# Performance work log

Measured on AMD Instinct MI355X. Metric: run time of the kernel, lower is better.

## Reference

```python
import jax, jax.numpy as jnp
import numpy as np

H = 64
VOCAB = 64
SLOTS = 8
EPS = 1e-5


def _layernorm(x, gamma, beta):
    mu = jnp.mean(x, axis=-1, keepdims=True)
    var = jnp.mean(jnp.square(x - mu), axis=-1, keepdims=True)
    return (x - mu) * jax.lax.rsqrt(var + EPS) * gamma + beta


def setup_inputs() -> dict:
    key = jax.random.key(0)
    ks = jax.random.split(key, 20)
    B, L = 1024, 2048
    s = 0.05
    inp = {
        "seq": jax.random.randint(ks[0], (B, L), 0, VOCAB, dtype=jnp.int64),
        "embed": jax.random.normal(ks[1], (VOCAB, H), jnp.float32) * s,
        "w1": jax.random.normal(ks[2], (2 * H, H), jnp.float32) * s,
        "b1": jnp.zeros((2 * H,), jnp.float32),
        "w2": jax.random.normal(ks[3], (H, 2 * H), jnp.float32) * s,
        "b2": jnp.zeros((H,), jnp.float32),
        "gamma": jnp.ones((H,), jnp.float32),
        "beta": jnp.zeros((H,), jnp.float32),
        "gate_w": jax.random.normal(ks[4], (1, H), jnp.float32) * s,
        "gate_b": jnp.zeros((1,), jnp.float32),
        "qi_w": jax.random.normal(ks[5], (H, H), jnp.float32) * s,
        "qi_b": jnp.zeros((H,), jnp.float32),
        "sk_w": jax.random.normal(ks[6], (H, H), jnp.float32) * s,
        "sk_b": jnp.zeros((H,), jnp.float32),
        "qr_w": jax.random.normal(ks[7], (H, H), jnp.float32) * s,
        "qr_b": jnp.zeros((H,), jnp.float32),
        "out_w": jax.random.normal(ks[8], (VOCAB, H), jnp.float32) * s,
        "out_b": jnp.zeros((VOCAB,), jnp.float32),
    }
    return inp


def reference(seq, embed, w1, b1, w2, b2, gamma, beta, gate_w, gate_b,
              qi_w, qi_b, sk_w, sk_b, qr_w, qr_b, out_w, out_b):
    # Encoder: embed -> FF residual -> LayerNorm
    h0 = embed[seq]                                  # [B, L, H]
    ff = jax.nn.relu(h0 @ w1.T + b1) @ w2.T + b2     # [B, L, H]
    h = _layernorm(h0 + ff, gamma, beta)             # [B, L, H]

    # Top-k gate over sequence -> gather memory slots
    scores = jnp.squeeze(h @ gate_w.T, -1) + gate_b[0]   # [B, L]
    _, idx = jax.lax.top_k(scores, SLOTS)                # [B, S]
    memory = jnp.take_along_axis(h, idx[:, :, None], axis=1)  # [B, S, H]

    scale = 1.0 / jnp.sqrt(jnp.float32(H))

    # Stage 1: initial read attention over slot keys
    q_init = h[:, -1, :] @ qi_w.T + qi_b                 # [B, H]
    slot_keys = memory @ sk_w.T + sk_b                   # [B, S, H]
    r_attn = jax.nn.softmax(jnp.einsum('bsh,bh->bs', slot_keys, q_init) * scale, axis=-1)
    read = jnp.einsum('bs,bsh->bh', r_attn, memory)
    q_refined = q_init + (read @ qr_w.T + qr_b)          # [B, H]

    # Stage 2: refined attention directly over memory
    attn = jax.nn.softmax(jnp.einsum('bsh,bh->bs', memory, q_refined) * scale, axis=-1)
    pooled = jnp.einsum('bs,bsh->bh', attn, memory)      # [B, H]
    return pooled @ out_w.T + out_b                      # [B, VOCAB]
```

## Files before the change

kernel.cpp:

```cpp
#include <hip/hip_runtime.h>
#include <hip/hip_bf16.h>

#define HD 64
#define LSEQ 2048
#define NBATCH 1024
#define NSLOTS 8

__global__ __launch_bounds__(128) void build_tables_kernel(
    const float* __restrict__ embed, const float* __restrict__ w1, const float* __restrict__ b1,
    const float* __restrict__ w2, const float* __restrict__ b2,
    const float* __restrict__ gamma, const float* __restrict__ beta,
    const float* __restrict__ gate_w, const float* __restrict__ gate_b,
    const float* __restrict__ qi_w, const float* __restrict__ qi_b,
    const float* __restrict__ sk_w, const float* __restrict__ sk_b,
    const float* __restrict__ qr_w, const float* __restrict__ out_w,
    float* __restrict__ h_table, float* __restrict__ qi_table, float* __restrict__ sk_table,
    float* __restrict__ qr_wT, float* __restrict__ out_wT, float* __restrict__ score)
{
    const int blk = blockIdx.x;
    const int tid = threadIdx.x;

    if (blk >= 64) {
        const float* src = (blk == 64) ? qr_w : out_w;
        float*       dst = (blk == 64) ? qr_wT : out_wT;
        for (int i = tid; i < HD * HD; i += 128) {
            int r = i >> 6, c = i & 63;
            dst[c * HD + r] = src[i];
        }
        return;
    }

    const int v = blk;
    __shared__ float E[HD];
    __shared__ float T1[2 * HD];
    __shared__ float Hrow[HD];

    if (tid < HD) E[tid] = embed[v * HD + tid];
    __syncthreads();

    {
        float t1 = b1[tid];
        const float* w1r = w1 + tid * HD;
        #pragma unroll 8
        for (int k = 0; k < HD; ++k) t1 = fmaf(E[k], w1r[k], t1);
        T1[tid] = fmaxf(t1, 0.0f);
    }
    __syncthreads();

    if (tid < HD) {
        float x = E[tid] + b2[tid];
        const float* w2r = w2 + tid * 2 * HD;
        #pragma unroll 8
        for (int j = 0; j < 2 * HD; ++j) x = fmaf(T1[j], w2r[j], x);

        float mu = x;
        #pragma unroll
        for (int off = 1; off < 64; off <<= 1) mu += __shfl_xor(mu, off);
        mu *= (1.0f / 64.0f);
        float d = x - mu;
        float var = d * d;
        #pragma unroll
        for (int off = 1; off < 64; off <<= 1) var += __shfl_xor(var, off);
        var *= (1.0f / 64.0f);
        float h = d * rsqrtf(var + 1e-5f) * gamma[tid] + beta[tid];
        Hrow[tid] = h;
        h_table[v * HD + tid] = h;

        float sc = h * gate_w[tid];
        #pragma unroll
        for (int off = 1; off < 64; off <<= 1) sc += __shfl_xor(sc, off);
        if (tid == 0) score[v] = sc + gate_b[0];
    }
    __syncthreads();

    {
        const int i = tid & 63;
        const float* W  = (tid < HD) ? qi_w : sk_w;
        const float* Bv = (tid < HD) ? qi_b : sk_b;
        float acc = Bv[i];
        const float* Wr = W + i * HD;
        #pragma unroll 8
        for (int k = 0; k < HD; ++k) acc = fmaf(Hrow[k], Wr[k], acc);
        float* dst = (tid < HD) ? qi_table : sk_table;
        dst[v * HD + i] = acc;
    }
}

__global__ __launch_bounds__(64) void sort_tokens_kernel(const float* __restrict__ score,
                                                         int* __restrict__ order)
{
    const int t = threadIdx.x;
    const float st = score[t];
    int rank = 0;
    for (int u = 0; u < 64; ++u) {
        float su = score[u];
        if (su > st || (su == st && u < t)) rank++;
    }
    order[rank] = t;
}

__global__ __launch_bounds__(64) void main_kernel(
    const int* __restrict__ seq,
    const float* __restrict__ h_table, const float* __restrict__ qi_table,
    const float* __restrict__ sk_table, const float* __restrict__ qr_wT,
    const float* __restrict__ qr_b, const float* __restrict__ out_wT,
    const float* __restrict__ out_b, const int* __restrict__ order,
    float* __restrict__ out)
{
    const int b    = blockIdx.x;
    const int lane = threadIdx.x;

    __shared__ int   hist[64];
    __shared__ int   slot_tok[NSLOTS];
    __shared__ float rbuf[64];

    hist[lane] = 0;
    __syncthreads();

    const int*  srow  = seq + (size_t)b * LSEQ;
    const int4* srow4 = (const int4*)srow;
    #pragma unroll
    for (int it = 0; it < LSEQ / 64 / 4; ++it) {
        int4 t4 = srow4[lane + it * 64];
        atomicAdd(&hist[t4.x], 1);
        atomicAdd(&hist[t4.y], 1);
        atomicAdd(&hist[t4.z], 1);
        atomicAdd(&hist[t4.w], 1);
    }
    __syncthreads();

    if (lane == 0) {
        int rem = NSLOTS, pos = 0;
        for (int t = 0; t < 64 && rem > 0; ++t) {
            int tok = order[t];
            int m = hist[tok];
            if (m > rem) m = rem;
            for (int i = 0; i < m; ++i) slot_tok[pos++] = tok;
            rem -= m;
        }
    }
    __syncthreads();

    int st[NSLOTS];
    #pragma unroll
    for (int s = 0; s < NSLOTS; ++s) st[s] = slot_tok[s];

    const int last = srow[LSEQ - 1];
    const float qk = qi_table[last * HD + lane];

    float mrow[NSLOTS], skrow[NSLOTS];
    #pragma unroll
    for (int s = 0; s < NSLOTS; ++s) {
        mrow[s]  = h_table[st[s] * HD + lane];
        skrow[s] = sk_table[st[s] * HD + lane];
    }

    const float scale = 0.125f;

    float p[NSLOTS];
    #pragma unroll
    for (int s = 0; s < NSLOTS; ++s) p[s] = skrow[s] * qk;
    #pragma unroll
    for (int off = 1; off < 64; off <<= 1) {
        #pragma unroll
        for (int s = 0; s < NSLOTS; ++s) p[s] += __shfl_xor(p[s], off);
    }
    {
        float mx = p[0];
        #pragma unroll
        for (int s = 1; s < NSLOTS; ++s) mx = fmaxf(mx, p[s]);
        float sum = 0.0f;
        #pragma unroll
        for (int s = 0; s < NSLOTS; ++s) { p[s] = __expf((p[s] - mx) * scale * 1.0f); }
        (void)sum;
    }
    #pragma unroll
    for (int s = 0; s < NSLOTS; ++s) p[s] = skrow[s] * qk;
    #pragma unroll
    for (int off = 1; off < 64; off <<= 1) {
        #pragma unroll
        for (int s = 0; s < NSLOTS; ++s) p[s] += __shfl_xor(p[s], off);
    }
    #pragma unroll
    for (int s = 0; s < NSLOTS; ++s) p[s] *= scale;
    float r[NSLOTS];
    {
        float mx = p[0];
        #pragma unroll
        for (int s = 1; s < NSLOTS; ++s) mx = fmaxf(mx, p[s]);
        float sum = 0.0f;
        #pragma unroll
        for (int s = 0; s < NSLOTS; ++s) { r[s] = expf(p[s] - mx); sum += r[s]; }
        float inv = 1.0f / sum;
        #pragma unroll
        for (int s = 0; s < NSLOTS; ++s) r[s] *= inv;
    }

    float readk = 0.0f;
    #pragma unroll
    for (int s = 0; s < NSLOTS; ++s) readk = fmaf(r[s], mrow[s], readk);

    rbuf[lane] = readk;
    __syncthreads();

    float qref = qk + qr_b[lane];
    #pragma unroll 4
    for (int j = 0; j < HD; ++j) qref = fmaf(rbuf[j], qr_wT[j * HD + lane], qref);

    float p2[NSLOTS];
    #pragma unroll
    for (int s = 0; s < NSLOTS; ++s) p2[s] = mrow[s] * qref;
    #pragma unroll
    for (int off = 1; off < 64; off <<= 1) {
        #pragma unroll
        for (int s = 0; s < NSLOTS; ++s) p2[s] += __shfl_xor(p2[s], off);
    }
    #pragma unroll
    for (int s = 0; s < NSLOTS; ++s) p2[s] *= scale;
    float a[NSLOTS];
    {
        float mx = p2[0];
        #pragma unroll
        for (int s = 1; s < NSLOTS; ++s) mx = fmaxf(mx, p2[s]);
        float sum = 0.0f;
        #pragma unroll
        for (int s = 0; s < NSLOTS; ++s) { a[s] = expf(p2[s] - mx); sum += a[s]; }
        float inv = 1.0f / sum;
        #pragma unroll
        for (int s = 0; s < NSLOTS; ++s) a[s] *= inv;
    }

    float pooledk = 0.0f;
    #pragma unroll
    for (int s = 0; s < NSLOTS; ++s) pooledk = fmaf(a[s], mrow[s], pooledk);

    __syncthreads();
    rbuf[lane] = pooledk;
    __syncthreads();

    float acc = out_b[lane];
    #pragma unroll 4
    for (int k = 0; k < HD; ++k) acc = fmaf(rbuf[k], out_wT[k * HD + lane], acc);

    out[(size_t)b * HD + lane] = acc;
}

extern "C" void kernel_launch(void* const* d_in, const int* in_sizes, int n_in,
                              void* d_out, int out_size, void* d_ws, size_t ws_size,
                              hipStream_t stream) {
    const int*   seq    = (const int*)  d_in[0];
    const float* embed  = (const float*)d_in[1];
    const float* w1     = (const float*)d_in[2];
    const float* b1     = (const float*)d_in[3];
    const float* w2     = (const float*)d_in[4];
    const float* b2     = (const float*)d_in[5];
    const float* gamma  = (const float*)d_in[6];
    const float* beta   = (const float*)d_in[7];
    const float* gate_w = (const float*)d_in[8];
    const float* gate_b = (const float*)d_in[9];
    const float* qi_w   = (const float*)d_in[10];
    const float* qi_b   = (const float*)d_in[11];
    const float* sk_w   = (const float*)d_in[12];
    const float* sk_b   = (const float*)d_in[13];
    const float* qr_w   = (const float*)d_in[14];
    const float* qr_b   = (const float*)d_in[15];
    const float* out_w  = (const float*)d_in[16];
    const float* out_b  = (const float*)d_in[17];

    float* ws = (float*)d_ws;
    float* h_table  = ws;
    float* qi_table = ws + 4096;
    float* sk_table = ws + 8192;
    float* qr_wT    = ws + 12288;
    float* out_wT   = ws + 16384;
    float* score    = ws + 20480;
    int*   order    = (int*)(ws + 20544);

    hipLaunchKernelGGL(build_tables_kernel, dim3(66), dim3(128), 0, stream,
                       embed, w1, b1, w2, b2, gamma, beta, gate_w, gate_b,
                       qi_w, qi_b, sk_w, sk_b, qr_w, out_w,
                       h_table, qi_table, sk_table, qr_wT, out_wT, score);

    hipLaunchKernelGGL(sort_tokens_kernel, dim3(1), dim3(64), 0, stream, score, order);

    hipLaunchKernelGGL(main_kernel, dim3(NBATCH), dim3(64), 0, stream,
                       seq, h_table, qi_table, sk_table, qr_wT, qr_b, out_wT, out_b,
                       order, (float*)d_out);
}
```

Before: 28.06 us.

## Fold token sort into main kernel, widen blocks, vectorize matvecs

Drops the separate sort kernel and the weight-transpose blocks. Each batch block now ranks the 64 token scores itself and places slots with a parallel prefix instead of a serial lane-0 loop. The main kernel uses 256 threads with per-wave privatized histograms and reads the whole sequence row in two int4 loads per thread. Matvecs read row-major weights as float4, and the dead duplicate softmax pass is removed. This saves one launch and serial work, at the cost of redundant per-block sorting and three idle waves during the attention phase.

```diff
diff --git a/kernel.cpp b/kernel.cpp
--- a/kernel.cpp
+++ b/kernel.cpp
@@ -13,46 +13,43 @@
     const float* __restrict__ gate_w, const float* __restrict__ gate_b,
     const float* __restrict__ qi_w, const float* __restrict__ qi_b,
     const float* __restrict__ sk_w, const float* __restrict__ sk_b,
-    const float* __restrict__ qr_w, const float* __restrict__ out_w,
     float* __restrict__ h_table, float* __restrict__ qi_table, float* __restrict__ sk_table,
-    float* __restrict__ qr_wT, float* __restrict__ out_wT, float* __restrict__ score)
+    float* __restrict__ score)
 {
-    const int blk = blockIdx.x;
+    const int v = blockIdx.x;
     const int tid = threadIdx.x;
 
-    if (blk >= 64) {
-        const float* src = (blk == 64) ? qr_w : out_w;
-        float*       dst = (blk == 64) ? qr_wT : out_wT;
-        for (int i = tid; i < HD * HD; i += 128) {
-            int r = i >> 6, c = i & 63;
-            dst[c * HD + r] = src[i];
-        }
-        return;
-    }
-
-    const int v = blk;
-    __shared__ float E[HD];
-    __shared__ float T1[2 * HD];
-    __shared__ float Hrow[HD];
+    __shared__ __align__(16) float E[HD];
+    __shared__ __align__(16) float T1[2 * HD];
+    __shared__ __align__(16) float Hrow[HD];
 
     if (tid < HD) E[tid] = embed[v * HD + tid];
     __syncthreads();
 
     {
-        float t1 = b1[tid];
-        const float* w1r = w1 + tid * HD;
-        #pragma unroll 8
-        for (int k = 0; k < HD; ++k) t1 = fmaf(E[k], w1r[k], t1);
-        T1[tid] = fmaxf(t1, 0.0f);
+        const float4* w1r = (const float4*)(w1 + tid * HD);
+        const float4* E4  = (const float4*)E;
+        float t = b1[tid];
+        #pragma unroll
+        for (int k = 0; k < HD / 4; ++k) {
+            float4 a = w1r[k], e = E4[k];
+            t = fmaf(a.x, e.x, t); t = fmaf(a.y, e.y, t);
+            t = fmaf(a.z, e.z, t); t = fmaf(a.w, e.w, t);
+        }
+        T1[tid] = fmaxf(t, 0.0f);
     }
     __syncthreads();
 
     if (tid < HD) {
+        const float4* w2r = (const float4*)(w2 + tid * 2 * HD);
+        const float4* T4  = (const float4*)T1;
         float x = E[tid] + b2[tid];
-        const float* w2r = w2 + tid * 2 * HD;
-        #pragma unroll 8
-        for (int j = 0; j < 2 * HD; ++j) x = fmaf(T1[j], w2r[j], x);
-
+        #pragma unroll
+        for (int j = 0; j < 2 * HD / 4; ++j) {
+            float4 a = w2r[j], t = T4[j];
+            x = fmaf(a.x, t.x, x); x = fmaf(a.y, t.y, x);
+            x = fmaf(a.z, t.z, x); x = fmaf(a.w, t.w, x);
+        }
         float mu = x;
         #pragma unroll
         for (int off = 1; off < 64; off <<= 1) mu += __shfl_xor(mu, off);
@@ -77,172 +74,174 @@
         const int i = tid & 63;
         const float* W  = (tid < HD) ? qi_w : sk_w;
         const float* Bv = (tid < HD) ? qi_b : sk_b;
+        const float4* Wr = (const float4*)(W + i * HD);
+        const float4* H4 = (const float4*)Hrow;
         float acc = Bv[i];
-        const float* Wr = W + i * HD;
-        #pragma unroll 8
-        for (int k = 0; k < HD; ++k) acc = fmaf(Hrow[k], Wr[k], acc);
+        #pragma unroll
+        for (int k = 0; k < HD / 4; ++k) {
+            float4 a = Wr[k], h = H4[k];
+            acc = fmaf(a.x, h.x, acc); acc = fmaf(a.y, h.y, acc);
+            acc = fmaf(a.z, h.z, acc); acc = fmaf(a.w, h.w, acc);
+        }
         float* dst = (tid < HD) ? qi_table : sk_table;
         dst[v * HD + i] = acc;
     }
 }
 
-__global__ __launch_bounds__(64) void sort_tokens_kernel(const float* __restrict__ score,
-                                                         int* __restrict__ order)
-{
-    const int t = threadIdx.x;
-    const float st = score[t];
-    int rank = 0;
-    for (int u = 0; u < 64; ++u) {
-        float su = score[u];
-        if (su > st || (su == st && u < t)) rank++;
-    }
-    order[rank] = t;
-}
-
-__global__ __launch_bounds__(64) void main_kernel(
+__global__ __launch_bounds__(256) void main_kernel(
     const int* __restrict__ seq,
     const float* __restrict__ h_table, const float* __restrict__ qi_table,
-    const float* __restrict__ sk_table, const float* __restrict__ qr_wT,
-    const float* __restrict__ qr_b, const float* __restrict__ out_wT,
-    const float* __restrict__ out_b, const int* __restrict__ order,
+    const float* __restrict__ sk_table,
+    const float* __restrict__ qr_w, const float* __restrict__ qr_b,
+    const float* __restrict__ out_w, const float* __restrict__ out_b,
+    const float* __restrict__ score,
     float* __restrict__ out)
 {
     const int b    = blockIdx.x;
-    const int lane = threadIdx.x;
-
-    __shared__ int   hist[64];
+    const int tid  = threadIdx.x;
+    const int w    = tid >> 6;
+    const int lane = tid & 63;
+
+    __shared__ int   hist[4][65];
     __shared__ int   slot_tok[NSLOTS];
-    __shared__ float rbuf[64];
-
-    hist[lane] = 0;
-    __syncthreads();
-
-    const int*  srow  = seq + (size_t)b * LSEQ;
-    const int4* srow4 = (const int4*)srow;
-    #pragma unroll
-    for (int it = 0; it < LSEQ / 64 / 4; ++it) {
-        int4 t4 = srow4[lane + it * 64];
-        atomicAdd(&hist[t4.x], 1);
-        atomicAdd(&hist[t4.y], 1);
-        atomicAdd(&hist[t4.z], 1);
-        atomicAdd(&hist[t4.w], 1);
-    }
-    __syncthreads();
-
-    if (lane == 0) {
-        int rem = NSLOTS, pos = 0;
-        for (int t = 0; t < 64 && rem > 0; ++t) {
-            int tok = order[t];
-            int m = hist[tok];
-            if (m > rem) m = rem;
-            for (int i = 0; i < m; ++i) slot_tok[pos++] = tok;
-            rem -= m;
-        }
-    }
-    __syncthreads();
-
-    int st[NSLOTS];
-    #pragma unroll
-    for (int s = 0; s < NSLOTS; ++s) st[s] = slot_tok[s];
-
-    const int last = srow[LSEQ - 1];
-    const float qk = qi_table[last * HD + lane];
-
-    float mrow[NSLOTS], skrow[NSLOTS];
-    #pragma unroll
-    for (int s = 0; s < NSLOTS; ++s) {
-        mrow[s]  = h_table[st[s] * HD + lane];
-        skrow[s] = sk_table[st[s] * HD + lane];
-    }
-
+    __shared__ float sbuf[64];
+    __shared__ int   order_s[64];
+    __shared__ int   cntb[64];
+    __shared__ int   last_s;
+    __shared__ __align__(16) float rbuf[64];
+
+    hist[w][lane] = 0;
+    if (tid < 64) sbuf[tid] = score[tid];
+
+    const int4* srow4 = (const int4*)(seq + (size_t)b * LSEQ);
+    int4 a0 = srow4[tid];
+    int4 a1 = srow4[256 + tid];
+    if (tid == 255) last_s = a1.w;
+    __syncthreads();
+
+    atomicAdd(&hist[w][a0.x], 1); atomicAdd(&hist[w][a0.y], 1);
+    atomicAdd(&hist[w][a0.z], 1); atomicAdd(&hist[w][a0.w], 1);
+    atomicAdd(&hist[w][a1.x], 1); atomicAdd(&hist[w][a1.y], 1);
+    atomicAdd(&hist[w][a1.z], 1); atomicAdd(&hist[w][a1.w], 1);
+    __syncthreads();
+
+    if (tid < 64) {
+        int cnt = hist[0][tid] + hist[1][tid] + hist[2][tid] + hist[3][tid];
+        float st = sbuf[tid];
+        int rank = 0;
+        for (int u = 0; u < 64; ++u) {
+            float su = sbuf[u];
+            if (su > st || (su == st && u < tid)) ++rank;
+        }
+        order_s[rank] = tid;
+        hist[0][tid] = cnt;
+    }
+    __syncthreads();
+
+    if (tid < 64) cntb[tid] = hist[0][order_s[tid]];
+    __syncthreads();
+
+    if (tid < 64) {
+        int cum = 0;
+        for (int u = 0; u < tid; ++u) cum += cntb[u];
+        int cnt = cntb[tid];
+        int tok = order_s[tid];
+        #pragma unroll
+        for (int s = 0; s < NSLOTS; ++s)
+            if (s >= cum && s < cum + cnt) slot_tok[s] = tok;
+    }
+    __syncthreads();
+
+    float qk = 0.0f;
+    float mrow[NSLOTS];
     const float scale = 0.125f;
 
-    float p[NSLOTS];
-    #pragma unroll
-    for (int s = 0; s < NSLOTS; ++s) p[s] = skrow[s] * qk;
-    #pragma unroll
-    for (int off = 1; off < 64; off <<= 1) {
-        #pragma unroll
-        for (int s = 0; s < NSLOTS; ++s) p[s] += __shfl_xor(p[s], off);
-    }
-    {
+    if (tid < 64) {
+        int st_[NSLOTS];
+        #pragma unroll
+        for (int s = 0; s < NSLOTS; ++s) st_[s] = slot_tok[s];
+
+        qk = qi_table[last_s * HD + lane];
+
+        float skrow[NSLOTS];
+        #pragma unroll
+        for (int s = 0; s < NSLOTS; ++s) {
+            mrow[s]  = h_table[st_[s] * HD + lane];
+            skrow[s] = sk_table[st_[s] * HD + lane];
+        }
+
+        float p[NSLOTS];
+        #pragma unroll
+        for (int s = 0; s < NSLOTS; ++s) p[s] = skrow[s] * qk;
+        #pragma unroll
+        for (int off = 1; off < 64; off <<= 1) {
+            #pragma unroll
+            for (int s = 0; s < NSLOTS; ++s) p[s] += __shfl_xor(p[s], off);
+        }
+        #pragma unroll
+        for (int s = 0; s < NSLOTS; ++s) p[s] *= scale;
         float mx = p[0];
         #pragma unroll
         for (int s = 1; s < NSLOTS; ++s) mx = fmaxf(mx, p[s]);
-        float sum = 0.0f;
-        #pragma unroll
-        for (int s = 0; s < NSLOTS; ++s) { p[s] = __expf((p[s] - mx) * scale * 1.0f); }
-        (void)sum;
-    }
-    #pragma unroll
-    for (int s = 0; s < NSLOTS; ++s) p[s] = skrow[s] * qk;
-    #pragma unroll
-    for (int off = 1; off < 64; off <<= 1) {
-        #pragma unroll
-        for (int s = 0; s < NSLOTS; ++s) p[s] += __shfl_xor(p[s], off);
-    }
-    #pragma unroll
-    for (int s = 0; s < NSLOTS; ++s) p[s] *= scale;
-    float r[NSLOTS];
-    {
-        float mx = p[0];
-        #pragma unroll
-        for (int s = 1; s < NSLOTS; ++s) mx = fmaxf(mx, p[s]);
-        float sum = 0.0f;
+        float sum = 0.0f, r[NSLOTS];
         #pragma unroll
         for (int s = 0; s < NSLOTS; ++s) { r[s] = expf(p[s] - mx); sum += r[s]; }
         float inv = 1.0f / sum;
-        #pragma unroll
-        for (int s = 0; s < NSLOTS; ++s) r[s] *= inv;
-    }
-
-    float readk = 0.0f;
-    #pragma unroll
-    for (int s = 0; s < NSLOTS; ++s) readk = fmaf(r[s], mrow[s], readk);
-
-    rbuf[lane] = readk;
-    __syncthreads();
-
-    float qref = qk + qr_b[lane];
-    #pragma unroll 4
-    for (int j = 0; j < HD; ++j) qref = fmaf(rbuf[j], qr_wT[j * HD + lane], qref);
-
-    float p2[NSLOTS];
-    #pragma unroll
-    for (int s = 0; s < NSLOTS; ++s) p2[s] = mrow[s] * qref;
-    #pragma unroll
-    for (int off = 1; off < 64; off <<= 1) {
-        #pragma unroll
-        for (int s = 0; s < NSLOTS; ++s) p2[s] += __shfl_xor(p2[s], off);
-    }
-    #pragma unroll
-    for (int s = 0; s < NSLOTS; ++s) p2[s] *= scale;
-    float a[NSLOTS];
-    {
+        float readk = 0.0f;
+        #pragma unroll
+        for (int s = 0; s < NSLOTS; ++s) readk = fmaf(r[s] * inv, mrow[s], readk);
+        rbuf[lane] = readk;
+    }
+    __syncthreads();
+
+    float qref = 0.0f;
+    if (tid < 64) {
+        qref = qk + qr_b[lane];
+        const float4* wr = (const float4*)(qr_w + lane * HD);
+        const float4* r4 = (const float4*)rbuf;
+        #pragma unroll
+        for (int j = 0; j < HD / 4; ++j) {
+            float4 a = wr[j], rv = r4[j];
+            qref = fmaf(a.x, rv.x, qref); qref = fmaf(a.y, rv.y, qref);
+            qref = fmaf(a.z, rv.z, qref); qref = fmaf(a.w, rv.w, qref);
+        }
+
+        float p2[NSLOTS];
+        #pragma unroll
+        for (int s = 0; s < NSLOTS; ++s) p2[s] = mrow[s] * qref;
+        #pragma unroll
+        for (int off = 1; off < 64; off <<= 1) {
+            #pragma unroll
+            for (int s = 0; s < NSLOTS; ++s) p2[s] += __shfl_xor(p2[s], off);
+        }
+        #pragma unroll
+        for (int s = 0; s < NSLOTS; ++s) p2[s] *= scale;
         float mx = p2[0];
         #pragma unroll
         for (int s = 1; s < NSLOTS; ++s) mx = fmaxf(mx, p2[s]);
-        float sum = 0.0f;
+        float sum = 0.0f, a[NSLOTS];
         #pragma unroll
         for (int s = 0; s < NSLOTS; ++s) { a[s] = expf(p2[s] - mx); sum += a[s]; }
         float inv = 1.0f / sum;
-        #pragma unroll
-        for (int s = 0; s < NSLOTS; ++s) a[s] *= inv;
-    }
-
-    float pooledk = 0.0f;
-    #pragma unroll
-    for (int s = 0; s < NSLOTS; ++s) pooledk = fmaf(a[s], mrow[s], pooledk);
-
-    __syncthreads();
-    rbuf[lane] = pooledk;
-    __syncthreads();
-
-    float acc = out_b[lane];
-    #pragma unroll 4
-    for (int k = 0; k < HD; ++k) acc = fmaf(rbuf[k], out_wT[k * HD + lane], acc);
-
-    out[(size_t)b * HD + lane] = acc;
+        float pooled = 0.0f;
+        #pragma unroll
+        for (int s = 0; s < NSLOTS; ++s) pooled = fmaf(a[s] * inv, mrow[s], pooled);
+        rbuf[lane] = pooled;
+    }
+    __syncthreads();
+
+    if (tid < 64) {
+        float acc = out_b[lane];
+        const float4* wr = (const float4*)(out_w + lane * HD);
+        const float4* r4 = (const float4*)rbuf;
+        #pragma unroll
+        for (int k = 0; k < HD / 4; ++k) {
+            float4 a = wr[k], rv = r4[k];
+            acc = fmaf(a.x, rv.x, acc); acc = fmaf(a.y, rv.y, acc);
+            acc = fmaf(a.z, rv.z, acc); acc = fmaf(a.w, rv.w, acc);
+        }
+        out[(size_t)b * HD + lane] = acc;
+    }
 }
 
 extern "C" void kernel_launch(void* const* d_in, const int* in_sizes, int n_in,
@@ -271,19 +270,14 @@
     float* h_table  = ws;
     float* qi_table = ws + 4096;
     float* sk_table = ws + 8192;
-    float* qr_wT    = ws + 12288;
-    float* out_wT   = ws + 16384;
-    float* score    = ws + 20480;
-    int*   order    = (int*)(ws + 20544);
-
-    hipLaunchKernelGGL(build_tables_kernel, dim3(66), dim3(128), 0, stream,
+    float* score    = ws + 12288;
+
+    hipLaunchKernelGGL(build_tables_kernel, dim3(64), dim3(128), 0, stream,
                        embed, w1, b1, w2, b2, gamma, beta, gate_w, gate_b,
-                       qi_w, qi_b, sk_w, sk_b, qr_w, out_w,
-                       h_table, qi_table, sk_table, qr_wT, out_wT, score);
-
-    hipLaunchKernelGGL(sort_tokens_kernel, dim3(1), dim3(64), 0, stream, score, order);
-
-    hipLaunchKernelGGL(main_kernel, dim3(NBATCH), dim3(64), 0, stream,
-                       seq, h_table, qi_table, sk_table, qr_wT, qr_b, out_wT, out_b,
-                       order, (float*)d_out);
+                       qi_w, qi_b, sk_w, sk_b,
+                       h_table, qi_table, sk_table, score);
+
+    hipLaunchKernelGGL(main_kernel, dim3(NBATCH), dim3(256), 0, stream,
+                       seq, h_table, qi_table, sk_table,
+                       qr_w, qr_b, out_w, out_b, score, (float*)d_out);
 }
```

Result: faster. 22.87 us (-18.5%).
